# Performance work log

Hardware: AMD Instinct MI355X
Metric: run time of the kernel (lower is better)

The kernel has to match this reference:

```python
import jax, jax.numpy as jnp
import numpy as np

NY, NU, NHIDDEN = 64, 64, 256
NHRZ, NBATCH = 1024, 128


def setup_inputs() -> dict:
    key = jax.random.key(0)
    ks = jax.random.split(key, 9)
    y0 = jax.random.normal(ks[0], (NBATCH, NY), dtype=jnp.float32)
    U = jax.random.normal(ks[1], (NHRZ, NBATCH, NU), dtype=jnp.float32)
    # parameters (match torch init: uniform(0,1) for continuous eigen params,
    # randn/sqrt(Nu) for B, Kaiming-uniform-ish for Linear layers)
    lmbd_cont_real = jax.random.uniform(ks[2], (NHIDDEN // 2,), dtype=jnp.float32)
    lmbd_cont_imag = jax.random.uniform(ks[3], (NHIDDEN // 2,), dtype=jnp.float32)
    B = jax.random.normal(ks[4], (NHIDDEN, NU), dtype=jnp.float32) / np.sqrt(NU)
    lim1 = 1.0 / np.sqrt(NY)
    W_y2x = jax.random.uniform(ks[5], (NHIDDEN, NY), dtype=jnp.float32, minval=-lim1, maxval=lim1)
    b_y2x = jax.random.uniform(ks[6], (NHIDDEN,), dtype=jnp.float32, minval=-lim1, maxval=lim1)
    lim2 = 1.0 / np.sqrt(NHIDDEN)
    W_x2y = jax.random.uniform(ks[7], (NY, NHIDDEN), dtype=jnp.float32, minval=-lim2, maxval=lim2)
    b_x2y = jax.random.uniform(ks[8], (NY,), dtype=jnp.float32, minval=-lim2, maxval=lim2)
    return {"y0": y0, "U": U, "lmbd_cont_real": lmbd_cont_real,
            "lmbd_cont_imag": lmbd_cont_imag, "B": B,
            "W_y2x": W_y2x, "b_y2x": b_y2x, "W_x2y": W_x2y, "b_x2y": b_x2y}


def reference(y0, U, lmbd_cont_real, lmbd_cont_imag, B, W_y2x, b_y2x, W_x2y, b_x2y):
    n = lmbd_cont_real.shape[0]  # Nhidden // 2
    r = jnp.exp(-jnp.abs(lmbd_cont_real))
    theta = (np.pi / 2.0) * lmbd_cont_imag
    lmbd_real = r * jnp.cos(theta)  # [n]
    lmbd_imag = r * jnp.sin(theta)  # [n]
    nf = jnp.sqrt(1.0 - jnp.exp(-2.0 * jnp.abs(lmbd_cont_real)))
    nf = jnp.concatenate([nf, nf])  # [Nhidden]
    # Bu[t,b,h] = (U @ B^T) * nf
    Bu = jnp.einsum('tbu,hu->tbh', U, B) * nf  # [Nhrz, Nbatch, Nhidden]
    x0 = y0 @ W_y2x.T + b_y2x  # [Nbatch, Nhidden]

    # x @ A^T with A = [[diag(lr), -diag(li)], [diag(li), diag(lr)]] is a
    # per-pair 2x2 rotation -> pure elementwise ops (same math, no dense matmul)
    def step(x, bu):
        x1, x2 = x[:, :n], x[:, n:]
        xn = jnp.concatenate([lmbd_real * x1 - lmbd_imag * x2,
                              lmbd_imag * x1 + lmbd_real * x2], axis=-1) + bu
        return xn, xn

    _, X = jax.lax.scan(step, x0, Bu)  # X: [Nhrz, Nbatch, Nhidden]
    Y = X @ W_x2y.T + b_x2y  # [Nhrz, Nbatch, Ny]
    return Y
```

## Files before the change

### kernel.cpp

```cpp
#include <hip/hip_runtime.h>
#include <hip/hip_bf16.h>
#include <stdint.h>

#define T_HRZ 1024
#define NBAT  128
#define NHID  256
#define NPAIR 128
#define NUIN  64
#define NYOUT 64
#define LCH   16
#define CCH   64
#define GCH   4
#define NGRP  16

#define WS_LAM   0
#define WS_LAML  256
#define WS_X0P   512
#define WS_WBU   33280
#define WS_WBY   41472
#define WS_SPUB  49664
#define WS_CNT   573952

#define X16_PITCH 264
#define XA_SB 136
#define XA_SK 552

typedef __attribute__((ext_vector_type(8))) short short8;
typedef __attribute__((ext_vector_type(4))) float float4v;

union Frag { short8 s8; unsigned int u32[4]; };

__device__ __forceinline__ unsigned int f2bf_bits(float x) {
  unsigned int u = __float_as_uint(x);
  return (u + 0x7fffu + ((u >> 16) & 1u)) >> 16;
}

__device__ __forceinline__ unsigned int pkbf(float a, float b) {
  __hip_bfloat162 h = __float22bfloat162_rn(make_float2(a, b));
  union { __hip_bfloat162 h2; unsigned int u; } cv; cv.h2 = h; return cv.u;
}

__global__ __launch_bounds__(256) void k_prep(
    const float* __restrict__ y0, const float* __restrict__ lrc,
    const float* __restrict__ lic, const float* __restrict__ Bm,
    const float* __restrict__ Wy2x, const float* __restrict__ by2x,
    const float* __restrict__ Wx2y, float* __restrict__ ws)
{
  int blk = blockIdx.x;
  int h = threadIdx.x;
  if (blk < NBAT) {
    __shared__ float y0s[NYOUT];
    if (h < NYOUT) y0s[h] = y0[blk * NYOUT + h];
    __syncthreads();
    float acc = by2x[h];
    const float* wr = Wy2x + h * NYOUT;
#pragma unroll 16
    for (int k = 0; k < NYOUT; ++k) acc += y0s[k] * wr[k];
    int j = h & (NPAIR - 1);
    int comp = h >> 7;
    ws[WS_X0P + (blk * NPAIR + j) * 2 + comp] = acc;
  } else if (blk == NBAT) {
    unsigned int* fl = (unsigned int*)(ws + WS_CNT);
    for (int i = h; i < NBAT * 16 + 1; i += 256) fl[i] = 0u;
    if (h < NPAIR) {
      float a  = fabsf(lrc[h]);
      float r  = expf(-a);
      float th = 1.5707963267948966f * lic[h];
      float lr = r * cosf(th);
      float li = r * sinf(th);
      ws[WS_LAM + h]         = lr;
      ws[WS_LAM + NPAIR + h] = li;
      float pr = lr, pi_ = li;
      for (int l = 1; l < LCH; ++l) {
        float nr = pr * lr - pi_ * li;
        float ni = pr * li + pi_ * lr;
        pr = nr; pi_ = ni;
      }
      ws[WS_LAML + h]         = pr;
      ws[WS_LAML + NPAIR + h] = pi_;
    }
  } else if (blk == NBAT + 1) {
    unsigned short* wbu = (unsigned short*)(ws + WS_WBU);
    for (int idx = h; idx < 16384; idx += 256) {
      int nt   = idx >> 10;
      int kk   = (idx >> 9) & 1;
      int lane = (idx >> 3) & 63;
      int jj   = idx & 7;
      int u  = kk * 32 + (lane >> 4) * 8 + jj;
      int hh = nt * 16 + (lane & 15);
      float a2 = fabsf(lrc[hh & (NPAIR - 1)]);
      float nf = sqrtf(1.f - expf(-2.f * a2));
      wbu[idx] = (unsigned short)f2bf_bits(Bm[hh * NUIN + u] * nf);
    }
  } else {
    unsigned short* wby = (unsigned short*)(ws + WS_WBY);
    for (int idx = h; idx < 16384; idx += 256) {
      int nt   = idx >> 12;
      int kk   = (idx >> 9) & 7;
      int lane = (idx >> 3) & 63;
      int jj   = idx & 7;
      int hh = kk * 32 + (lane >> 4) * 8 + jj;
      int y  = nt * 16 + (lane & 15);
      wby[idx] = (unsigned short)f2bf_bits(Wx2y[y * NHID + hh]);
    }
  }
}

__global__ __launch_bounds__(128, 4) void k_main(
    const float* __restrict__ U, const float* __restrict__ bx2y,
    float* __restrict__ out, float* __restrict__ ws)
{
  __shared__ unsigned short X16s[LCH * X16_PITCH];
  __shared__ unsigned short XAs[8 * XA_SK];
  __shared__ unsigned int vid_s;
  int tid = threadIdx.x, wave = tid >> 6, lane = tid & 63;
  int l15 = lane & 15, q = lane >> 4;

  unsigned int* cnt = (unsigned int*)(ws + WS_CNT);
  if (tid == 0) vid_s = atomicAdd(cnt + NBAT * 16, 1u);
  __syncthreads();
  unsigned int vid = vid_s;
  int g = (int)(vid >> 7);
  int b = (int)(vid & (NBAT - 1));

  int j = tid;
  float lr = ws[WS_LAM + j],  li = ws[WS_LAM + NPAIR + j];

  const short8* wbu = (const short8*)(ws + WS_WBU);
  float4v z = {0.f, 0.f, 0.f, 0.f};

  float S1 = 0.f, S2 = 0.f;

#pragma unroll
  for (int k = 0; k < GCH; ++k) {
    int c = g * GCH + k;
    const float* urow = U + ((size_t)(c * LCH + l15) * NBAT + b) * NUIN;
    Frag afr[2];
#pragma unroll
    for (int kk = 0; kk < 2; ++kk) {
      int u0 = kk * 32 + q * 8;
      float4 va = *(const float4*)(urow + u0);
      float4 vb = *(const float4*)(urow + u0 + 4);
      afr[kk].u32[0] = pkbf(va.x, va.y);
      afr[kk].u32[1] = pkbf(va.z, va.w);
      afr[kk].u32[2] = pkbf(vb.x, vb.y);
      afr[kk].u32[3] = pkbf(vb.z, vb.w);
    }
    float4v acc[8];
#pragma unroll
    for (int n = 0; n < 8; ++n) acc[n] = z;
#pragma unroll
    for (int n = 0; n < 8; ++n) {
      int nt = wave * 8 + n;
      acc[n] = __builtin_amdgcn_mfma_f32_16x16x32_bf16(afr[0].s8, wbu[(nt * 2 + 0) * 64 + lane], acc[n], 0, 0, 0);
      acc[n] = __builtin_amdgcn_mfma_f32_16x16x32_bf16(afr[1].s8, wbu[(nt * 2 + 1) * 64 + lane], acc[n], 0, 0, 0);
    }
#pragma unroll
    for (int n = 0; n < 8; ++n) {
      int hh = (wave * 8 + n) * 16 + l15;
      int off = (hh & 127) * 2 + (hh >> 7);
#pragma unroll
      for (int r = 0; r < 4; ++r)
        X16s[(q * 4 + r) * X16_PITCH + off] = (unsigned short)f2bf_bits(acc[n][r]);
    }
    __syncthreads();
#pragma unroll
    for (int l = 0; l < LCH; ++l) {
      unsigned int pkv = *(const unsigned int*)(X16s + l * X16_PITCH + j * 2);
      float v1 = __uint_as_float(pkv << 16);
      float v2 = __uint_as_float(pkv & 0xffff0000u);
      float n1 = lr * S1 - li * S2 + v1;
      float n2 = li * S1 + lr * S2 + v2;
      S1 = n1; S2 = n2;
    }
    __syncthreads();
  }

  unsigned long long* spub = (unsigned long long*)(ws + WS_SPUB);
  const size_t cs = (size_t)NBAT * NPAIR;
  size_t o0 = (size_t)b * NPAIR + j;
  if (g < NGRP - 1) {
    unsigned long long pv = ((unsigned long long)__float_as_uint(S2) << 32)
                          |  (unsigned long long)__float_as_uint(S1);
    __hip_atomic_store(spub + (size_t)g * cs + o0, pv,
                       __ATOMIC_RELAXED, __HIP_MEMORY_SCOPE_AGENT);
  }
  __syncthreads();
  if (tid == 0 && g < NGRP - 1)
    atomicOr(cnt + b * 16, 1u << g);

  float L16r = ws[WS_LAML + j], L16i = ws[WS_LAML + NPAIR + j];
  float L32r = L16r * L16r - L16i * L16i, L32i = 2.f * L16r * L16i;
  float L64r = L32r * L32r - L32i * L32i, L64i = 2.f * L32r * L32i;

  float e1, e2;
  e1 = ws[WS_X0P + (b * NPAIR + j) * 2 + 0];
  e2 = ws[WS_X0P + (b * NPAIR + j) * 2 + 1];
  if (g > 0) {
    unsigned int need = (1u << g) - 1u;
    if (tid == 0) {
      while ((__hip_atomic_load(cnt + b * 16, __ATOMIC_RELAXED,
                                __HIP_MEMORY_SCOPE_AGENT) & need) != need)
        __builtin_amdgcn_s_sleep(1);
    }
    __syncthreads();
    unsigned long long sv[NGRP - 1];
#pragma unroll
    for (int g2 = 0; g2 < NGRP - 1; ++g2)
      if (g2 < g)
        sv[g2] = __hip_atomic_load(spub + (size_t)g2 * cs + o0,
                                   __ATOMIC_RELAXED, __HIP_MEMORY_SCOPE_AGENT);
#pragma unroll
    for (int g2 = 0; g2 < NGRP - 1; ++g2)
      if (g2 < g) {
        float s1 = __uint_as_float((unsigned int)sv[g2]);
        float s2 = __uint_as_float((unsigned int)(sv[g2] >> 32));
        float n1 = L64r * e1 - L64i * e2 + s1;
        float n2 = L64i * e1 + L64r * e2 + s2;
        e1 = n1; e2 = n2;
      }
  }

  const short8* wby = (const short8*)(ws + WS_WBY);
  int base1 = (j >> 5) * XA_SK       + ((j >> 3) & 3) * XA_SB + (j & 7);
  int base2 = ((j >> 5) + 4) * XA_SK + ((j >> 3) & 3) * XA_SB + (j & 7);
  float x1 = e1, x2 = e2;
  float bias0 = bx2y[(wave * 2 + 0) * 16 + l15];
  float bias1 = bx2y[(wave * 2 + 1) * 16 + l15];
#pragma unroll
  for (int k = 0; k < GCH; ++k) {
    int c = g * GCH + k;
    const float* urow = U + ((size_t)(c * LCH + l15) * NBAT + b) * NUIN;
    Frag afr[2];
#pragma unroll
    for (int kk = 0; kk < 2; ++kk) {
      int u0 = kk * 32 + q * 8;
      float4 va = *(const float4*)(urow + u0);
      float4 vb = *(const float4*)(urow + u0 + 4);
      afr[kk].u32[0] = pkbf(va.x, va.y);
      afr[kk].u32[1] = pkbf(va.z, va.w);
      afr[kk].u32[2] = pkbf(vb.x, vb.y);
      afr[kk].u32[3] = pkbf(vb.z, vb.w);
    }
    float4v acc[8];
#pragma unroll
    for (int n = 0; n < 8; ++n) acc[n] = z;
#pragma unroll
    for (int n = 0; n < 8; ++n) {
      int nt = wave * 8 + n;
      acc[n] = __builtin_amdgcn_mfma_f32_16x16x32_bf16(afr[0].s8, wbu[(nt * 2 + 0) * 64 + lane], acc[n], 0, 0, 0);
      acc[n] = __builtin_amdgcn_mfma_f32_16x16x32_bf16(afr[1].s8, wbu[(nt * 2 + 1) * 64 + lane], acc[n], 0, 0, 0);
    }
#pragma unroll
    for (int n = 0; n < 8; ++n) {
      int hh = (wave * 8 + n) * 16 + l15;
      int off = (hh & 127) * 2 + (hh >> 7);
#pragma unroll
      for (int r = 0; r < 4; ++r)
        X16s[(q * 4 + r) * X16_PITCH + off] = (unsigned short)f2bf_bits(acc[n][r]);
    }
    __syncthreads();
#pragma unroll
    for (int l = 0; l < LCH; ++l) {
      unsigned int pkv = *(const unsigned int*)(X16s + l * X16_PITCH + j * 2);
      float v1 = __uint_as_float(pkv << 16);
      float v2 = __uint_as_float(pkv & 0xffff0000u);
      float n1 = lr * x1 - li * x2 + v1;
      float n2 = li * x1 + lr * x2 + v2;
      x1 = n1; x2 = n2;
      XAs[base1 + l * 8] = (unsigned short)f2bf_bits(x1);
      XAs[base2 + l * 8] = (unsigned short)f2bf_bits(x2);
    }
    __syncthreads();
    float4v acc0 = z, acc1 = z;
    int nt0 = wave * 2, nt1 = nt0 + 1;
#pragma unroll
    for (int kk = 0; kk < 8; ++kk) {
      short8 a = *(const short8*)(XAs + kk * XA_SK + q * XA_SB + l15 * 8);
      acc0 = __builtin_amdgcn_mfma_f32_16x16x32_bf16(a, wby[(nt0 * 8 + kk) * 64 + lane], acc0, 0, 0, 0);
      acc1 = __builtin_amdgcn_mfma_f32_16x16x32_bf16(a, wby[(nt1 * 8 + kk) * 64 + lane], acc1, 0, 0, 0);
    }
#pragma unroll
    for (int r = 0; r < 4; ++r) {
      int row = q * 4 + r;
      size_t o = ((size_t)(c * LCH + row) * NBAT + b) * NYOUT;
      out[o + nt0 * 16 + l15] = acc0[r] + bias0;
      out[o + nt1 * 16 + l15] = acc1[r] + bias1;
    }
  }
}

extern "C" void kernel_launch(void* const* d_in, const int* in_sizes, int n_in,
                              void* d_out, int out_size, void* d_ws, size_t ws_size,
                              hipStream_t stream) {
  (void)in_sizes; (void)n_in; (void)out_size; (void)ws_size;
  const float* y0   = (const float*)d_in[0];
  const float* U    = (const float*)d_in[1];
  const float* lrc  = (const float*)d_in[2];
  const float* lic  = (const float*)d_in[3];
  const float* Bm   = (const float*)d_in[4];
  const float* Wy2x = (const float*)d_in[5];
  const float* by2x = (const float*)d_in[6];
  const float* Wx2y = (const float*)d_in[7];
  const float* bx2y = (const float*)d_in[8];
  float* out = (float*)d_out;
  float* ws  = (float*)d_ws;

  k_prep<<<dim3(NBAT + 3), 256, 0, stream>>>(y0, lrc, lic, Bm, Wy2x, by2x, Wx2y, ws);
  k_main<<<dim3(NGRP * NBAT), 128, 0, stream>>>(U, bx2y, out, ws);
}
```

Baseline: 175.2 us.

## Split fused chunked scan into two kernels instead of cross-block spin-wait

Replaces the single persistent kernel, which took ticket-ordered block IDs and made blocks spin on atomic flags for earlier groups' chunk states, with two launches. Pass 1 computes per-group local scan end states and writes them to workspace. Pass 2 combines the prefix states and recomputes the scan plus output projection. This removes atomics, spin-waits and flag clearing, at the cost of an extra launch, a kernel boundary, and redone Bu work in pass 1 that can no longer overlap with pass 2.

New measurement: 152.0 us. -13.3%, faster.

```diff
diff --git a/kernel.cpp b/kernel.cpp
--- a/kernel.cpp
+++ b/kernel.cpp
@@ -18,8 +18,7 @@
 #define WS_X0P   512
 #define WS_WBU   33280
 #define WS_WBY   41472
-#define WS_SPUB  49664
-#define WS_CNT   573952
+#define WS_S     49664
 
 #define X16_PITCH 264
 #define XA_SB 136
@@ -60,8 +59,6 @@
     int comp = h >> 7;
     ws[WS_X0P + (blk * NPAIR + j) * 2 + comp] = acc;
   } else if (blk == NBAT) {
-    unsigned int* fl = (unsigned int*)(ws + WS_CNT);
-    for (int i = h; i < NBAT * 16 + 1; i += 256) fl[i] = 0u;
     if (h < NPAIR) {
       float a  = fabsf(lrc[h]);
       float r  = expf(-a);
@@ -106,29 +103,19 @@
   }
 }
 
-__global__ __launch_bounds__(128, 4) void k_main(
-    const float* __restrict__ U, const float* __restrict__ bx2y,
-    float* __restrict__ out, float* __restrict__ ws)
+__global__ __launch_bounds__(128, 4) void k_pass1(
+    const float* __restrict__ U, float* __restrict__ ws)
 {
   __shared__ unsigned short X16s[LCH * X16_PITCH];
-  __shared__ unsigned short XAs[8 * XA_SK];
-  __shared__ unsigned int vid_s;
   int tid = threadIdx.x, wave = tid >> 6, lane = tid & 63;
   int l15 = lane & 15, q = lane >> 4;
-
-  unsigned int* cnt = (unsigned int*)(ws + WS_CNT);
-  if (tid == 0) vid_s = atomicAdd(cnt + NBAT * 16, 1u);
-  __syncthreads();
-  unsigned int vid = vid_s;
-  int g = (int)(vid >> 7);
-  int b = (int)(vid & (NBAT - 1));
+  int b = blockIdx.x, g = blockIdx.y;
 
   int j = tid;
-  float lr = ws[WS_LAM + j],  li = ws[WS_LAM + NPAIR + j];
+  float lr = ws[WS_LAM + j], li = ws[WS_LAM + NPAIR + j];
 
   const short8* wbu = (const short8*)(ws + WS_WBU);
   float4v z = {0.f, 0.f, 0.f, 0.f};
-
   float S1 = 0.f, S2 = 0.f;
 
 #pragma unroll
@@ -173,60 +160,51 @@
       float n2 = li * S1 + lr * S2 + v2;
       S1 = n1; S2 = n2;
     }
-    __syncthreads();
-  }
-
-  unsigned long long* spub = (unsigned long long*)(ws + WS_SPUB);
-  const size_t cs = (size_t)NBAT * NPAIR;
-  size_t o0 = (size_t)b * NPAIR + j;
-  if (g < NGRP - 1) {
-    unsigned long long pv = ((unsigned long long)__float_as_uint(S2) << 32)
-                          |  (unsigned long long)__float_as_uint(S1);
-    __hip_atomic_store(spub + (size_t)g * cs + o0, pv,
-                       __ATOMIC_RELAXED, __HIP_MEMORY_SCOPE_AGENT);
-  }
-  __syncthreads();
-  if (tid == 0 && g < NGRP - 1)
-    atomicOr(cnt + b * 16, 1u << g);
-
+    if (k < GCH - 1) __syncthreads();
+  }
+
+  ((float2*)(ws + WS_S))[((size_t)g * NBAT + b) * NPAIR + j] = make_float2(S1, S2);
+}
+
+__global__ __launch_bounds__(128, 4) void k_pass2(
+    const float* __restrict__ U, const float* __restrict__ bx2y,
+    float* __restrict__ out, float* __restrict__ ws)
+{
+  __shared__ unsigned short X16s[LCH * X16_PITCH];
+  __shared__ unsigned short XAs[8 * XA_SK];
+  int tid = threadIdx.x, wave = tid >> 6, lane = tid & 63;
+  int l15 = lane & 15, q = lane >> 4;
+  int b = blockIdx.x, g = blockIdx.y;
+
+  int j = tid;
+  float lr = ws[WS_LAM + j], li = ws[WS_LAM + NPAIR + j];
   float L16r = ws[WS_LAML + j], L16i = ws[WS_LAML + NPAIR + j];
   float L32r = L16r * L16r - L16i * L16i, L32i = 2.f * L16r * L16i;
   float L64r = L32r * L32r - L32i * L32i, L64i = 2.f * L32r * L32i;
 
-  float e1, e2;
-  e1 = ws[WS_X0P + (b * NPAIR + j) * 2 + 0];
-  e2 = ws[WS_X0P + (b * NPAIR + j) * 2 + 1];
-  if (g > 0) {
-    unsigned int need = (1u << g) - 1u;
-    if (tid == 0) {
-      while ((__hip_atomic_load(cnt + b * 16, __ATOMIC_RELAXED,
-                                __HIP_MEMORY_SCOPE_AGENT) & need) != need)
-        __builtin_amdgcn_s_sleep(1);
-    }
-    __syncthreads();
-    unsigned long long sv[NGRP - 1];
-#pragma unroll
-    for (int g2 = 0; g2 < NGRP - 1; ++g2)
-      if (g2 < g)
-        sv[g2] = __hip_atomic_load(spub + (size_t)g2 * cs + o0,
-                                   __ATOMIC_RELAXED, __HIP_MEMORY_SCOPE_AGENT);
+  float e1 = ws[WS_X0P + (b * NPAIR + j) * 2 + 0];
+  float e2 = ws[WS_X0P + (b * NPAIR + j) * 2 + 1];
+  {
+    const float2* sp = (const float2*)(ws + WS_S);
 #pragma unroll
     for (int g2 = 0; g2 < NGRP - 1; ++g2)
       if (g2 < g) {
-        float s1 = __uint_as_float((unsigned int)sv[g2]);
-        float s2 = __uint_as_float((unsigned int)(sv[g2] >> 32));
-        float n1 = L64r * e1 - L64i * e2 + s1;
-        float n2 = L64i * e1 + L64r * e2 + s2;
+        float2 s = sp[((size_t)g2 * NBAT + b) * NPAIR + j];
+        float n1 = L64r * e1 - L64i * e2 + s.x;
+        float n2 = L64i * e1 + L64r * e2 + s.y;
         e1 = n1; e2 = n2;
       }
   }
 
+  const short8* wbu = (const short8*)(ws + WS_WBU);
   const short8* wby = (const short8*)(ws + WS_WBY);
+  float4v z = {0.f, 0.f, 0.f, 0.f};
   int base1 = (j >> 5) * XA_SK       + ((j >> 3) & 3) * XA_SB + (j & 7);
   int base2 = ((j >> 5) + 4) * XA_SK + ((j >> 3) & 3) * XA_SB + (j & 7);
   float x1 = e1, x2 = e2;
   float bias0 = bx2y[(wave * 2 + 0) * 16 + l15];
   float bias1 = bx2y[(wave * 2 + 1) * 16 + l15];
+
 #pragma unroll
   for (int k = 0; k < GCH; ++k) {
     int c = g * GCH + k;
@@ -307,5 +285,6 @@
   float* ws  = (float*)d_ws;
 
   k_prep<<<dim3(NBAT + 3), 256, 0, stream>>>(y0, lrc, lic, Bm, Wy2x, by2x, Wx2y, ws);
-  k_main<<<dim3(NGRP * NBAT), 128, 0, stream>>>(U, bx2y, out, ws);
-}
+  k_pass1<<<dim3(NBAT, NGRP - 1), 128, 0, stream>>>(U, ws);
+  k_pass2<<<dim3(NBAT, NGRP), 128, 0, stream>>>(U, bx2y, out, ws);
+}
```
